# Performance work log

Hardware: AMD Instinct MI355X
Metric: run time of the kernel (lower is better)

The kernel has to match this reference:

```python
import jax, jax.numpy as jnp
import numpy as np

N_NODES = 50000
N_EDGES = 800000
H = 128            # node_hidden_size
T = 2              # num_prop_rounds


def setup_inputs() -> dict:
    key = jax.random.key(0)
    ks = jax.random.split(key, 10)
    hv = jax.random.normal(ks[0], (N_NODES, H), dtype=jnp.float32)
    he = jax.random.normal(ks[1], (N_EDGES, 1), dtype=jnp.float32)
    src = jax.random.randint(ks[2], (N_EDGES,), 0, N_NODES, dtype=jnp.int32)
    dst = jax.random.randint(ks[3], (N_EDGES,), 0, N_NODES, dtype=jnp.int32)
    # per-round params, stacked on leading T axis; small scale to avoid gate saturation
    W_msg = jax.random.normal(ks[4], (T, 2 * H, 2 * H + 1), dtype=jnp.float32) * 0.05
    b_msg = jax.random.normal(ks[5], (T, 2 * H), dtype=jnp.float32) * 0.05
    W_ih = jax.random.normal(ks[6], (T, 3 * H, 2 * H), dtype=jnp.float32) * 0.05
    W_hh = jax.random.normal(ks[7], (T, 3 * H, H), dtype=jnp.float32) * 0.05
    b_ih = jax.random.normal(ks[8], (T, 3 * H), dtype=jnp.float32) * 0.05
    b_hh = jax.random.normal(ks[9], (T, 3 * H), dtype=jnp.float32) * 0.05
    return dict(hv=hv, he=he, src=src, dst=dst, W_msg=W_msg, b_msg=b_msg,
                W_ih=W_ih, W_hh=W_hh, b_ih=b_ih, b_hh=b_hh)


def _gru_cell(x, h, W_ih, W_hh, b_ih, b_hh):
    # torch.nn.GRUCell math
    gi = x @ W_ih.T + b_ih          # [N, 3H]
    gh = h @ W_hh.T + b_hh          # [N, 3H]
    i_r, i_z, i_n = jnp.split(gi, 3, axis=1)
    h_r, h_z, h_n = jnp.split(gh, 3, axis=1)
    r = jax.nn.sigmoid(i_r + h_r)
    z = jax.nn.sigmoid(i_z + h_z)
    n = jnp.tanh(i_n + r * h_n)
    return (1.0 - z) * n + z * h


def reference(hv, he, src, dst, W_msg, b_msg, W_ih, W_hh, b_ih, b_hh):
    n_nodes = hv.shape[0]
    for t in range(T):
        # per-edge message input: concat([hv_dst, hv_src, he])  [E, 2H+1]
        msg_in = jnp.concatenate([hv[dst], hv[src], he], axis=1)
        edge_act = msg_in @ W_msg[t].T + b_msg[t]          # [E, 2H]
        # ragged sum-reduce over incoming edges (deg-0 nodes get zeros)
        a = jax.ops.segment_sum(edge_act, dst, num_segments=n_nodes)  # [N, 2H]
        hv = _gru_cell(a, hv, W_ih[t], W_hh[t], b_ih[t], b_hh[t])
    return hv
```

## Files before the change

### kernel.cpp

```cpp
#include <hip/hip_runtime.h>
#include <cstdint>
#include <cstddef>

#define N_NODES 50000
#define N_EDGES 800000
#define HDIM 128
#define TROUNDS 2
#define NTILES 3125
#define PACK_PER_T (416 * 64)
#define MAXDEG 64
#define NBUK 196
#define BCAP 4608
#define BCE 2048
#define NBC ((N_EDGES + BCE - 1) / BCE)

typedef __attribute__((ext_vector_type(8))) _Float16 half8v;
typedef __attribute__((ext_vector_type(2))) _Float16 half2v;
typedef __attribute__((ext_vector_type(4))) float f32x4;
typedef unsigned short ushort_t;
typedef unsigned long long u64;

#define GLD_LDS(gp, lp)                                                        \
  __builtin_amdgcn_global_load_lds(                                            \
      (__attribute__((address_space(1))) const void*)(gp),                     \
      (__attribute__((address_space(3))) void*)(lp), 16, 0, 0)

static __device__ __forceinline__ float sigmoidf_(float x) {
  return 1.0f / (1.0f + __expf(-x));
}
static __device__ __forceinline__ float tanhf_(float x) {
  float xc = fminf(15.0f, fmaxf(-15.0f, x));
  float a = __expf(2.0f * xc);
  return (a - 1.0f) / (a + 1.0f);
}
static __device__ __forceinline__ float f16bits2f(uint32_t hb) {
  ushort_t u = (ushort_t)hb;
  _Float16 h;
  __builtin_memcpy(&h, &u, 2);
  return (float)h;
}

__global__ void pack_all(const float* __restrict__ Wmsg, const float* __restrict__ Wih,
                         const float* __restrict__ Whh, _Float16* __restrict__ W1p,
                         _Float16* __restrict__ W2p, float* __restrict__ we) {
  int g = blockIdx.x * blockDim.x + threadIdx.x;
  if (g < TROUNDS * 256) {
    int t = g >> 8, j = g & 255;
    we[g] = Wmsg[((size_t)t * 256 + j) * 257 + 256];
  }
  if (g >= TROUNDS * PACK_PER_T) return;
  int t = g / PACK_PER_T;
  int r = g % PACK_PER_T;
  int lane = r & 63;
  int fr = r >> 6;
  const float* srcp;
  _Float16* dstp;
  if (fr < 128) {
    int jt = fr >> 3, kt = fr & 7;
    int j = jt * 16 + (lane & 15);
    int k = kt * 32 + ((lane >> 4) << 3);
    srcp = Wmsg + (size_t)t * 256 * 257 + (size_t)j * 257 + k;
    dstp = W1p + ((size_t)t * 128 + fr) * 512 + lane * 8;
  } else {
    int fr2 = fr - 128;
    int chunk = fr2 / 12, idx = fr2 % 12;
    int jt = chunk / 3, pp = chunk % 3;
    int j = pp * 128 + jt * 16 + (lane & 15);
    int k;
    if (idx < 8) {
      k = idx * 32 + ((lane >> 4) << 3);
      srcp = Wih + (size_t)t * 384 * 256 + (size_t)j * 256 + k;
    } else {
      k = (idx - 8) * 32 + ((lane >> 4) << 3);
      srcp = Whh + (size_t)t * 384 * 128 + (size_t)j * 128 + k;
    }
    dstp = W2p + ((size_t)t * 288 + fr2) * 512 + lane * 8;
  }
  #pragma unroll
  for (int e = 0; e < 8; ++e) dstp[e] = (_Float16)srcp[e];
}

__global__ void cast_hv(const float* __restrict__ hv, _Float16* __restrict__ hvh) {
  int i = blockIdx.x * blockDim.x + threadIdx.x;
  if (i >= N_NODES * HDIM / 4) return;
  float4 v = reinterpret_cast<const float4*>(hv)[i];
  half2v o0, o1;
  o0[0] = (_Float16)v.x; o0[1] = (_Float16)v.y;
  o1[0] = (_Float16)v.z; o1[1] = (_Float16)v.w;
  reinterpret_cast<half2v*>(hvh)[i * 2] = o0;
  reinterpret_cast<half2v*>(hvh)[i * 2 + 1] = o1;
}

__global__ __launch_bounds__(256) void bin_count(
    const int* __restrict__ src, const int* __restrict__ dst,
    const float* __restrict__ he, int* __restrict__ bcur, u64* __restrict__ barr) {
  __shared__ int hist[256];
  __shared__ int incl[256];
  __shared__ int cur[256];
  __shared__ int gbase[256];
  __shared__ u64 staged[BCE];
  const int tid = threadIdx.x;
  const int e0 = blockIdx.x * BCE;
  const int tot = min(BCE, N_EDGES - e0);

  hist[tid] = 0;
  __syncthreads();

  u64 rec[BCE / 256];
  int nmine = 0;
  #pragma unroll
  for (int q = 0; q < BCE / 256; ++q) {
    int e = e0 + q * 256 + tid;
    if (e < N_EDGES) {
      uint32_t d = (uint32_t)dst[e];
      uint32_t s = (uint32_t)src[e];
      _Float16 hh = (_Float16)he[e];
      ushort_t hb;
      __builtin_memcpy(&hb, &hh, 2);
      rec[nmine] = ((u64)d << 32) | ((u64)hb << 16) | (u64)s;
      atomicAdd(&hist[d >> 8], 1);
      ++nmine;
    }
  }
  __syncthreads();

  incl[tid] = hist[tid];
  __syncthreads();
  for (int off = 1; off < 256; off <<= 1) {
    int v = incl[tid];
    int a = (tid >= off) ? incl[tid - off] : 0;
    __syncthreads();
    incl[tid] = v + a;
    __syncthreads();
  }
  cur[tid] = incl[tid] - hist[tid];
  __syncthreads();

  for (int q = 0; q < nmine; ++q) {
    int b = (int)(rec[q] >> 40);
    int pos = atomicAdd(&cur[b], 1);
    staged[pos] = rec[q];
  }
  if (tid < NBUK && hist[tid] > 0) gbase[tid] = atomicAdd(&bcur[tid], hist[tid]);
  __syncthreads();

  for (int i = tid; i < tot; i += 256) {
    u64 r = staged[i];
    int b = (int)(r >> 40);
    int excl = incl[b] - hist[b];
    barr[(size_t)b * BCAP + gbase[b] + (i - excl)] = r;
  }
}

__global__ __launch_bounds__(256) void bin_place(
    const int* __restrict__ bcur, const u64* __restrict__ barr,
    uint32_t* __restrict__ csr, int* __restrict__ deg_i) {
  __shared__ int lcnt[256];
  const int b = blockIdx.x;
  const int tid = threadIdx.x;
  const int cnt = bcur[b];
  lcnt[tid] = 0;
  __syncthreads();
  const u64* bp = barr + (size_t)b * BCAP;
  for (int i = tid; i < cnt; i += 256) {
    u64 r = bp[i];
    int d = (int)((r >> 32) & 0xffffu);
    int slot = atomicAdd(&lcnt[d & 255], 1);
    if (slot < MAXDEG) csr[(size_t)d * MAXDEG + slot] = (uint32_t)r;
  }
  __syncthreads();
  int node = b * 256 + tid;
  if (node < N_NODES) deg_i[node] = min(lcnt[tid], MAXDEG);
}

__global__ void gather_h(const _Float16* __restrict__ hvh, const int* __restrict__ deg_i,
                         const uint32_t* __restrict__ csr, _Float16* __restrict__ S_h,
                         float* __restrict__ hsum, float* __restrict__ deg_f, int n) {
  int wid = (int)((blockIdx.x * blockDim.x + threadIdx.x) >> 6);
  int lane = threadIdx.x & 63;
  if (wid >= n) return;
  int deg = deg_i[wid];
  uint32_t ent = (lane < deg) ? csr[(size_t)wid * MAXDEG + lane] : 0u;
  float a0 = 0.f, a1 = 0.f, hs = 0.f;
  int k = 0;
  for (; k + 7 < deg; k += 8) {
    uint32_t ee[8];
    #pragma unroll
    for (int q = 0; q < 8; ++q) ee[q] = __shfl(ent, k + q);
    half2v vv[8];
    #pragma unroll
    for (int q = 0; q < 8; ++q)
      vv[q] = *reinterpret_cast<const half2v*>(hvh + (size_t)(ee[q] & 0xffffu) * HDIM + lane * 2);
    #pragma unroll
    for (int q = 0; q < 8; ++q) {
      a0 += (float)vv[q][0];
      a1 += (float)vv[q][1];
      hs += f16bits2f(ee[q] >> 16);
    }
  }
  for (; k < deg; ++k) {
    uint32_t e0 = __shfl(ent, k);
    half2v v0 = *reinterpret_cast<const half2v*>(hvh + (size_t)(e0 & 0xffffu) * HDIM + lane * 2);
    a0 += (float)v0[0];
    a1 += (float)v0[1];
    hs += f16bits2f(e0 >> 16);
  }
  half2v o;
  o[0] = (_Float16)a0;
  o[1] = (_Float16)a1;
  *reinterpret_cast<half2v*>(S_h + (size_t)wid * HDIM + lane * 2) = o;
  if (lane == 0) hsum[wid] = hs;
  if (lane == 1) deg_f[wid] = (float)deg;
}

__global__ __launch_bounds__(256, 4) void u1_kernel(
    const float* __restrict__ hv, const _Float16* __restrict__ S_h,
    const float* __restrict__ deg_f, const float* __restrict__ hsum,
    const _Float16* __restrict__ W1p, const float* __restrict__ we,
    const float* __restrict__ bmsg, _Float16* __restrict__ a_out) {
  __shared__ _Float16 buf[2][8 * 512];
  const int tid = threadIdx.x;
  const int wv = tid >> 6, lane = tid & 63;
  const int tile = blockIdx.x * 4 + wv;
  const bool act = (tile < NTILES);
  const int rowA = tile * 16 + (lane & 15);
  const int koff = (lane >> 4) * 8;
  const int m0 = (lane >> 4) * 4;

  {
    const _Float16* g = W1p + (size_t)(wv * 2) * 512 + lane * 8;
    #pragma unroll
    for (int i = 0; i < 2; ++i) GLD_LDS(g + i * 512, &buf[0][(wv * 2 + i) * 512]);
  }

  half8v x[8];
  float degs[4], hss[4];
  if (act) {
    float deg = deg_f[rowA];
    const float* hrow = hv + (size_t)rowA * HDIM;
    #pragma unroll
    for (int kt = 0; kt < 4; ++kt) {
      const float* sp = hrow + kt * 32 + koff;
      #pragma unroll
      for (int e = 0; e < 8; ++e) x[kt][e] = (_Float16)(sp[e] * deg);
    }
    const _Float16* srow = S_h + (size_t)rowA * HDIM + koff;
    #pragma unroll
    for (int kt = 0; kt < 4; ++kt)
      x[4 + kt] = *reinterpret_cast<const half8v*>(srow + kt * 32);
    #pragma unroll
    for (int rr = 0; rr < 4; ++rr) {
      degs[rr] = deg_f[tile * 16 + m0 + rr];
      hss[rr] = hsum[tile * 16 + m0 + rr];
    }
  }

  #pragma unroll 1
  for (int jt = 0; jt < 16; ++jt) {
    __syncthreads();
    if (jt < 15) {
      const _Float16* g = W1p + (size_t)(jt + 1) * 4096 + (size_t)(wv * 2) * 512 + lane * 8;
      #pragma unroll
      for (int i = 0; i < 2; ++i) GLD_LDS(g + i * 512, &buf[(jt + 1) & 1][(wv * 2 + i) * 512]);
    }
    const _Float16* B = &buf[jt & 1][0];
    f32x4 acc = {0.f, 0.f, 0.f, 0.f};
    #pragma unroll
    for (int kt = 0; kt < 8; ++kt) {
      half8v b = *reinterpret_cast<const half8v*>(B + (size_t)kt * 512 + lane * 8);
      acc = __builtin_amdgcn_mfma_f32_16x16x32_f16(x[kt], b, acc, 0, 0, 0);
    }
    if (act) {
      int j = jt * 16 + (lane & 15);
      float bm = bmsg[j], w = we[j];
      #pragma unroll
      for (int rr = 0; rr < 4; ++rr)
        a_out[(size_t)(tile * 16 + m0 + rr) * 256 + j] =
            (_Float16)(acc[rr] + degs[rr] * bm + hss[rr] * w);
    }
  }
}

__global__ __launch_bounds__(256, 4) void u2_kernel(
    const float* __restrict__ hv_in, const _Float16* __restrict__ a_in,
    const _Float16* __restrict__ W2p, const float* __restrict__ bih,
    const float* __restrict__ bhh, float* __restrict__ hv_out,
    _Float16* __restrict__ hvh_out) {
  __shared__ _Float16 buf[2][12 * 512];
  const int tid = threadIdx.x;
  const int wv = tid >> 6, lane = tid & 63;
  const int tile = blockIdx.x * 4 + wv;
  const bool act = (tile < NTILES);
  const int rowA = tile * 16 + (lane & 15);
  const int koff = (lane >> 4) * 8;
  const int m0 = (lane >> 4) * 4;

  auto stage = [&](int n) {
    const _Float16* g = W2p + (size_t)n * 6144 + (size_t)(wv * 3) * 512 + lane * 8;
    _Float16* l = &buf[n & 1][(wv * 3) * 512];
    #pragma unroll
    for (int i = 0; i < 3; ++i) GLD_LDS(g + i * 512, l + i * 512);
  };

  stage(0);

  half8v a8[8], h4[4];
  if (act) {
    const _Float16* ar = a_in + (size_t)rowA * 256 + koff;
    #pragma unroll
    for (int kt = 0; kt < 8; ++kt)
      a8[kt] = *reinterpret_cast<const half8v*>(ar + kt * 32);
    const float* hr = hv_in + (size_t)rowA * HDIM + koff;
    #pragma unroll
    for (int kt = 0; kt < 4; ++kt) {
      #pragma unroll
      for (int e = 0; e < 8; ++e) h4[kt][e] = (_Float16)hr[kt * 32 + e];
    }
  }

  auto compute = [&](const _Float16* B, f32x4& ai, f32x4& ag) {
    ai = (f32x4){0.f, 0.f, 0.f, 0.f};
    ag = (f32x4){0.f, 0.f, 0.f, 0.f};
    #pragma unroll
    for (int kt = 0; kt < 8; ++kt) {
      half8v b = *reinterpret_cast<const half8v*>(B + (size_t)kt * 512 + lane * 8);
      ai = __builtin_amdgcn_mfma_f32_16x16x32_f16(a8[kt], b, ai, 0, 0, 0);
    }
    #pragma unroll
    for (int kt = 0; kt < 4; ++kt) {
      half8v b = *reinterpret_cast<const half8v*>(B + (size_t)(8 + kt) * 512 + lane * 8);
      ag = __builtin_amdgcn_mfma_f32_16x16x32_f16(h4[kt], b, ag, 0, 0, 0);
    }
  };

  f32x4 rreg, zreg, ai, ag;
  #pragma unroll 1
  for (int jt = 0; jt < 8; ++jt) {
    const int c0 = jt * 3;
    const int fcol = jt * 16 + (lane & 15);
    __syncthreads();
    stage(c0 + 1);
    compute(&buf[c0 & 1][0], ai, ag);
    if (act) {
      float bi = bih[fcol], bq = bhh[fcol];
      #pragma unroll
      for (int rr = 0; rr < 4; ++rr) rreg[rr] = sigmoidf_(ai[rr] + bi + ag[rr] + bq);
    }
    __syncthreads();
    stage(c0 + 2);
    compute(&buf[(c0 + 1) & 1][0], ai, ag);
    if (act) {
      float bi = bih[128 + fcol], bq = bhh[128 + fcol];
      #pragma unroll
      for (int rr = 0; rr < 4; ++rr) zreg[rr] = sigmoidf_(ai[rr] + bi + ag[rr] + bq);
    }
    __syncthreads();
    if (jt < 7) stage(c0 + 3);
    compute(&buf[(c0 + 2) & 1][0], ai, ag);
    if (act) {
      float bi = bih[256 + fcol], bq = bhh[256 + fcol];
      #pragma unroll
      for (int rr = 0; rr < 4; ++rr) {
        int node = tile * 16 + m0 + rr;
        float n = tanhf_(ai[rr] + bi + rreg[rr] * (ag[rr] + bq));
        float h = hv_in[(size_t)node * HDIM + fcol];
        float hn = (1.f - zreg[rr]) * n + zreg[rr] * h;
        hv_out[(size_t)node * HDIM + fcol] = hn;
        hvh_out[(size_t)node * HDIM + fcol] = (_Float16)hn;
      }
    }
  }
}

extern "C" void kernel_launch(void* const* d_in, const int* in_sizes, int n_in,
                              void* d_out, int out_size, void* d_ws, size_t ws_size,
                              hipStream_t stream) {
  const float* hv   = (const float*)d_in[0];
  const float* he   = (const float*)d_in[1];
  const int*   src  = (const int*)d_in[2];
  const int*   dst  = (const int*)d_in[3];
  const float* Wmsg = (const float*)d_in[4];
  const float* bmsg = (const float*)d_in[5];
  const float* Wih  = (const float*)d_in[6];
  const float* Whh  = (const float*)d_in[7];
  const float* bih  = (const float*)d_in[8];
  const float* bhh  = (const float*)d_in[9];

  char* p = (char*)d_ws;
  auto alloc = [&](size_t bytes) { char* r = p; p += (bytes + 255) & ~(size_t)255; return r; };
  _Float16* S_h   = (_Float16*)alloc((size_t)N_NODES * HDIM * 2);
  _Float16* a_buf = (_Float16*)alloc((size_t)N_NODES * 256 * 2);
  _Float16* hvh   = (_Float16*)alloc((size_t)N_NODES * HDIM * 2);
  float*    deg_f = (float*)alloc((size_t)N_NODES * 4);
  float*    hsum  = (float*)alloc((size_t)N_NODES * 4);
  float*    we    = (float*)alloc((size_t)TROUNDS * 256 * 4);
  const size_t W1PT = (size_t)128 * 512;
  const size_t W2PT = (size_t)288 * 512;
  _Float16* W1p = (_Float16*)alloc(TROUNDS * W1PT * 2);
  _Float16* W2p = (_Float16*)alloc(TROUNDS * W2PT * 2);
  int*      deg_i = (int*)alloc((size_t)N_NODES * 4);
  int*      bcur  = (int*)alloc((size_t)NBUK * 4);
  u64*      barr  = (u64*)alloc((size_t)NBUK * BCAP * 8);
  uint32_t* csr   = (uint32_t*)alloc((size_t)N_NODES * MAXDEG * 4);

  hipMemsetAsync(bcur, 0, (size_t)NBUK * 4, stream);

  pack_all<<<(TROUNDS * PACK_PER_T + 255) / 256, 256, 0, stream>>>(Wmsg, Wih, Whh, W1p, W2p, we);
  cast_hv<<<(N_NODES * HDIM / 4 + 255) / 256, 256, 0, stream>>>(hv, hvh);
  bin_count<<<NBC, 256, 0, stream>>>(src, dst, he, bcur, barr);
  bin_place<<<NBUK, 256, 0, stream>>>(bcur, barr, csr, deg_i);

  const float* hcur = hv;
  float* outp = (float*)d_out;
  const int ugrid = (NTILES + 3) / 4;
  for (int t = 0; t < TROUNDS; ++t) {
    gather_h<<<(N_NODES + 3) / 4, 256, 0, stream>>>(hvh, deg_i, csr, S_h, hsum, deg_f, N_NODES);
    u1_kernel<<<ugrid, 256, 0, stream>>>(
        hcur, S_h, deg_f, hsum, W1p + (size_t)t * W1PT,
        we + (size_t)t * 256, bmsg + (size_t)t * 256, a_buf);
    u2_kernel<<<ugrid, 256, 0, stream>>>(
        hcur, a_buf, W2p + (size_t)t * W2PT,
        bih + (size_t)t * 384, bhh + (size_t)t * 384, outp, hvh);
    hcur = outp;
  }
  (void)in_sizes; (void)n_in; (void)out_size; (void)ws_size;
}
```

Before: 225.1 us.

## Triple-buffer weight staging in GRU GEMM kernels and read fp16 hidden state

Both u1 and u2 move from double to triple buffering of the packed weight tiles in LDS. Each step now prefetches two chunks ahead and uses one explicit vmcnt wait plus a barrier instead of a full __syncthreads, so more global-to-LDS copy time overlaps the MFMA work. u2 also loads the hidden state as fp16 from the hvh copy rather than converting fp32 hv in registers, which cuts load traffic. The fixed vmcnt counts ignore interleaved global stores and loads, so they may wait longer than needed. LDS use per block also grows, which can limit occupancy.

Result: slower. 239.8 us (+6.5%).

```diff
diff --git a/kernel.cpp b/kernel.cpp
--- a/kernel.cpp
+++ b/kernel.cpp
@@ -218,7 +218,7 @@
     const float* __restrict__ deg_f, const float* __restrict__ hsum,
     const _Float16* __restrict__ W1p, const float* __restrict__ we,
     const float* __restrict__ bmsg, _Float16* __restrict__ a_out) {
-  __shared__ _Float16 buf[2][8 * 512];
+  __shared__ _Float16 buf[3][8 * 512];
   const int tid = threadIdx.x;
   const int wv = tid >> 6, lane = tid & 63;
   const int tile = blockIdx.x * 4 + wv;
@@ -227,12 +227,6 @@
   const int koff = (lane >> 4) * 8;
   const int m0 = (lane >> 4) * 4;
 
-  {
-    const _Float16* g = W1p + (size_t)(wv * 2) * 512 + lane * 8;
-    #pragma unroll
-    for (int i = 0; i < 2; ++i) GLD_LDS(g + i * 512, &buf[0][(wv * 2 + i) * 512]);
-  }
-
   half8v x[8];
   float degs[4], hss[4];
   if (act) {
@@ -255,15 +249,22 @@
     }
   }
 
+  auto stage1 = [&](int c) {
+    const _Float16* g = W1p + (size_t)c * 4096 + (size_t)(wv * 2) * 512 + lane * 8;
+    _Float16* l = &buf[c % 3][(wv * 2) * 512];
+    #pragma unroll
+    for (int i = 0; i < 2; ++i) GLD_LDS(g + i * 512, l + i * 512);
+  };
+  stage1(0);
+  stage1(1);
+
   #pragma unroll 1
   for (int jt = 0; jt < 16; ++jt) {
-    __syncthreads();
-    if (jt < 15) {
-      const _Float16* g = W1p + (size_t)(jt + 1) * 4096 + (size_t)(wv * 2) * 512 + lane * 8;
-      #pragma unroll
-      for (int i = 0; i < 2; ++i) GLD_LDS(g + i * 512, &buf[(jt + 1) & 1][(wv * 2 + i) * 512]);
-    }
-    const _Float16* B = &buf[jt & 1][0];
+    asm volatile("s_waitcnt vmcnt(2)" ::: "memory");
+    __builtin_amdgcn_s_barrier();
+    __builtin_amdgcn_sched_barrier(0);
+    if (jt < 14) stage1(jt + 2);
+    const _Float16* B = &buf[jt % 3][0];
     f32x4 acc = {0.f, 0.f, 0.f, 0.f};
     #pragma unroll
     for (int kt = 0; kt < 8; ++kt) {
@@ -283,10 +284,10 @@
 
 __global__ __launch_bounds__(256, 4) void u2_kernel(
     const float* __restrict__ hv_in, const _Float16* __restrict__ a_in,
-    const _Float16* __restrict__ W2p, const float* __restrict__ bih,
-    const float* __restrict__ bhh, float* __restrict__ hv_out,
-    _Float16* __restrict__ hvh_out) {
-  __shared__ _Float16 buf[2][12 * 512];
+    const _Float16* __restrict__ hvh_in, const _Float16* __restrict__ W2p,
+    const float* __restrict__ bih, const float* __restrict__ bhh,
+    float* __restrict__ hv_out, _Float16* __restrict__ hvh_out) {
+  __shared__ _Float16 buf[3][12 * 512];
   const int tid = threadIdx.x;
   const int wv = tid >> 6, lane = tid & 63;
   const int tile = blockIdx.x * 4 + wv;
@@ -295,28 +296,26 @@
   const int koff = (lane >> 4) * 8;
   const int m0 = (lane >> 4) * 4;
 
-  auto stage = [&](int n) {
-    const _Float16* g = W2p + (size_t)n * 6144 + (size_t)(wv * 3) * 512 + lane * 8;
-    _Float16* l = &buf[n & 1][(wv * 3) * 512];
-    #pragma unroll
-    for (int i = 0; i < 3; ++i) GLD_LDS(g + i * 512, l + i * 512);
-  };
-
-  stage(0);
-
   half8v a8[8], h4[4];
   if (act) {
     const _Float16* ar = a_in + (size_t)rowA * 256 + koff;
     #pragma unroll
     for (int kt = 0; kt < 8; ++kt)
       a8[kt] = *reinterpret_cast<const half8v*>(ar + kt * 32);
-    const float* hr = hv_in + (size_t)rowA * HDIM + koff;
-    #pragma unroll
-    for (int kt = 0; kt < 4; ++kt) {
-      #pragma unroll
-      for (int e = 0; e < 8; ++e) h4[kt][e] = (_Float16)hr[kt * 32 + e];
-    }
-  }
+    const _Float16* hr = hvh_in + (size_t)rowA * HDIM + koff;
+    #pragma unroll
+    for (int kt = 0; kt < 4; ++kt)
+      h4[kt] = *reinterpret_cast<const half8v*>(hr + kt * 32);
+  }
+
+  auto stage = [&](int c) {
+    const _Float16* g = W2p + (size_t)c * 6144 + (size_t)(wv * 3) * 512 + lane * 8;
+    _Float16* l = &buf[c % 3][(wv * 3) * 512];
+    #pragma unroll
+    for (int i = 0; i < 3; ++i) GLD_LDS(g + i * 512, l + i * 512);
+  };
+  stage(0);
+  stage(1);
 
   auto compute = [&](const _Float16* B, f32x4& ai, f32x4& ag) {
     ai = (f32x4){0.f, 0.f, 0.f, 0.f};
@@ -336,37 +335,36 @@
   f32x4 rreg, zreg, ai, ag;
   #pragma unroll 1
   for (int jt = 0; jt < 8; ++jt) {
-    const int c0 = jt * 3;
     const int fcol = jt * 16 + (lane & 15);
-    __syncthreads();
-    stage(c0 + 1);
-    compute(&buf[c0 & 1][0], ai, ag);
-    if (act) {
-      float bi = bih[fcol], bq = bhh[fcol];
-      #pragma unroll
-      for (int rr = 0; rr < 4; ++rr) rreg[rr] = sigmoidf_(ai[rr] + bi + ag[rr] + bq);
-    }
-    __syncthreads();
-    stage(c0 + 2);
-    compute(&buf[(c0 + 1) & 1][0], ai, ag);
-    if (act) {
-      float bi = bih[128 + fcol], bq = bhh[128 + fcol];
-      #pragma unroll
-      for (int rr = 0; rr < 4; ++rr) zreg[rr] = sigmoidf_(ai[rr] + bi + ag[rr] + bq);
-    }
-    __syncthreads();
-    if (jt < 7) stage(c0 + 3);
-    compute(&buf[(c0 + 2) & 1][0], ai, ag);
-    if (act) {
-      float bi = bih[256 + fcol], bq = bhh[256 + fcol];
-      #pragma unroll
-      for (int rr = 0; rr < 4; ++rr) {
-        int node = tile * 16 + m0 + rr;
-        float n = tanhf_(ai[rr] + bi + rreg[rr] * (ag[rr] + bq));
-        float h = hv_in[(size_t)node * HDIM + fcol];
-        float hn = (1.f - zreg[rr]) * n + zreg[rr] * h;
-        hv_out[(size_t)node * HDIM + fcol] = hn;
-        hvh_out[(size_t)node * HDIM + fcol] = (_Float16)hn;
+    #pragma unroll 1
+    for (int p = 0; p < 3; ++p) {
+      const int c = jt * 3 + p;
+      asm volatile("s_waitcnt vmcnt(3)" ::: "memory");
+      __builtin_amdgcn_s_barrier();
+      __builtin_amdgcn_sched_barrier(0);
+      if (c < 22) stage(c + 2);
+      compute(&buf[c % 3][0], ai, ag);
+      if (act) {
+        if (p == 0) {
+          float bi = bih[fcol], bq = bhh[fcol];
+          #pragma unroll
+          for (int rr = 0; rr < 4; ++rr) rreg[rr] = sigmoidf_(ai[rr] + bi + ag[rr] + bq);
+        } else if (p == 1) {
+          float bi = bih[128 + fcol], bq = bhh[128 + fcol];
+          #pragma unroll
+          for (int rr = 0; rr < 4; ++rr) zreg[rr] = sigmoidf_(ai[rr] + bi + ag[rr] + bq);
+        } else {
+          float bi = bih[256 + fcol], bq = bhh[256 + fcol];
+          #pragma unroll
+          for (int rr = 0; rr < 4; ++rr) {
+            int node = tile * 16 + m0 + rr;
+            float n = tanhf_(ai[rr] + bi + rreg[rr] * (ag[rr] + bq));
+            float h = hv_in[(size_t)node * HDIM + fcol];
+            float hn = (1.f - zreg[rr]) * n + zreg[rr] * h;
+            hv_out[(size_t)node * HDIM + fcol] = hn;
+            hvh_out[(size_t)node * HDIM + fcol] = (_Float16)hn;
+          }
+        }
       }
     }
   }
@@ -419,7 +417,7 @@
         hcur, S_h, deg_f, hsum, W1p + (size_t)t * W1PT,
         we + (size_t)t * 256, bmsg + (size_t)t * 256, a_buf);
     u2_kernel<<<ugrid, 256, 0, stream>>>(
-        hcur, a_buf, W2p + (size_t)t * W2PT,
+        hcur, a_buf, hvh, W2p + (size_t)t * W2PT,
         bih + (size_t)t * 384, bhh + (size_t)t * 384, outp, hvh);
     hcur = outp;
   }
```
